# Performance work log

Hardware: AMD Instinct MI355X
Metric: run time of the kernel (lower is better)

Reference implementation:

```python
import jax, jax.numpy as jnp
import numpy as np

S = 14
B = 2
L_COORD = 5.0
L_NOOBJ = 0.5


def setup_inputs() -> dict:
    key = jax.random.key(0)
    k1, k2, k3 = jax.random.split(key, 3)
    N = 4096
    D = B * 5 + 20  # 30 channels
    pred = jax.random.uniform(k1, (N, S, S, D), dtype=jnp.float32)
    targ = jax.random.uniform(k2, (N, S, S, D), dtype=jnp.float32)
    # objectness channel of the target must be exactly 0 or 1 (loss masks on ==1 / ==0)
    obj = (jax.random.uniform(k3, (N, S, S)) < 0.15).astype(jnp.float32)
    targ = targ.at[..., 4].set(obj)
    return {"pred_tensor": pred, "target_tensor": targ}


def _yolo_loss(pred_tensor, target_tensor):
    N = pred_tensor.shape[0]
    dt = pred_tensor.dtype
    m = (target_tensor[..., 4] == 1).astype(dt)      # [N,S,S] obj mask
    nm = (target_tensor[..., 4] == 0).astype(dt)     # [N,S,S] noobj mask

    tb = target_tensor[..., :5]                                   # [N,S,S,5]
    pb = pred_tensor[..., :5 * B].reshape(N, S, S, B, 5)          # [N,S,S,B,5]

    # cell offsets: x-offset = column index j, y-offset = row index i
    ii, jj = jnp.meshgrid(jnp.arange(S, dtype=dt), jnp.arange(S, dtype=dt), indexing="ij")
    off = jnp.stack([jj, ii], axis=-1)                            # [S,S,2] = (ox, oy)

    def to_xyxy(box, off):
        # xy is scaled by 1/S, wh is NOT (faithful to the torch code)
        xy = box[..., 0:2] / S + off / S
        half = 0.5 * box[..., 2:4]
        return jnp.concatenate([xy - half, xy + half], axis=-1)

    t_xyxy = to_xyxy(tb, off)                                     # [N,S,S,4]
    p_xyxy = to_xyxy(pb, off[:, :, None, :])                      # [N,S,S,B,4]

    # per-cell IoU of target box vs each of the B predicted boxes
    lt = jnp.maximum(t_xyxy[..., None, :2], p_xyxy[..., :2])      # [N,S,S,B,2]
    rb = jnp.minimum(t_xyxy[..., None, 2:], p_xyxy[..., 2:])
    wh = jnp.clip(rb - lt, 0.0)
    inter = wh[..., 0] * wh[..., 1]                               # [N,S,S,B]
    area_t = (tb[..., 2] * tb[..., 3])[..., None]                 # [N,S,S,1]
    area_p = pb[..., 2] * pb[..., 3]                              # [N,S,S,B]
    iou = inter / (area_t + area_p - inter)                       # [N,S,S,B]

    k = jnp.argmax(iou, axis=-1)                                  # [N,S,S]
    best = jnp.take_along_axis(pb, k[..., None, None], axis=3)[..., 0, :]  # [N,S,S,5]
    best_iou = jnp.take_along_axis(iou, k[..., None], axis=-1)[..., 0]     # [N,S,S]

    loss_xy = jnp.sum(m[..., None] * (tb[..., :2] - best[..., :2]) ** 2) * L_COORD / N
    loss_wh = jnp.sum(m[..., None] * (jnp.sqrt(tb[..., 2:4]) - jnp.sqrt(best[..., 2:4])) ** 2) * L_COORD / N
    loss_Cobj = jnp.sum(m * (best_iou - best[..., 4]) ** 2) / N

    conf_sq = pb[..., 4] ** 2                                     # [N,S,S,B]
    is_best = (k[..., None] == jnp.arange(B)).astype(dt)          # [N,S,S,B]
    loss_Cnoobj = (jnp.sum(nm[..., None] * conf_sq)
                   + jnp.sum(m[..., None] * (1.0 - is_best) * conf_sq)) * L_NOOBJ / N

    loss_class = jnp.sum(m[..., None] * (target_tensor[..., 5 * B:] - pred_tensor[..., 5 * B:]) ** 2) / N

    loss_res = loss_xy + loss_wh + loss_Cobj + loss_Cnoobj + loss_class
    return (loss_res, loss_xy, loss_wh, loss_Cobj, loss_Cnoobj, loss_class)


@jax.jit
def reference(pred_tensor, target_tensor):
    return _yolo_loss(pred_tensor, target_tensor)
```

## Files before the change

kernel.cpp:

```cpp
#include <hip/hip_runtime.h>


constexpr int SS  = 14;
constexpr int TPB = 64;
constexpr int CPT = 64;
constexpr int TFL = CPT * 30;

typedef unsigned int u32;
typedef __attribute__((address_space(3))) u32 lds_u32;
typedef __attribute__((address_space(1))) const u32 glb_u32;

__device__ __forceinline__ void box_loss(
    float p0, float p1, float p2, float p3, float p4,
    float p5, float p6, float p7, float p8, float p9,
    float t0, float t1, float t2, float t3, float t4,
    float offx, float offy,
    float& s0, float& s1, float& s2, float& s3, float& m_out)
{
    float m  = (t4 == 1.0f) ? 1.0f : 0.0f;
    float nm = (t4 == 0.0f) ? 1.0f : 0.0f;
    m_out = m;

    const float S = 14.0f;
    float tcx = t0 / S + offx / S;
    float tcy = t1 / S + offy / S;
    float thw = 0.5f * t2, thh = 0.5f * t3;
    float tx0 = tcx - thw, ty0 = tcy - thh;
    float tx1 = tcx + thw, ty1 = tcy + thh;
    float area_t = t2 * t3;

    float iou0, iou1;
    {
        float cx = p0 / S + offx / S, cy = p1 / S + offy / S;
        float hw = 0.5f * p2, hh = 0.5f * p3;
        float x0 = cx - hw, y0 = cy - hh, x1 = cx + hw, y1 = cy + hh;
        float wx = fmaxf(fminf(tx1, x1) - fmaxf(tx0, x0), 0.f);
        float wy = fmaxf(fminf(ty1, y1) - fmaxf(ty0, y0), 0.f);
        float inter = wx * wy;
        iou0 = inter / (area_t + p2 * p3 - inter);
    }
    {
        float cx = p5 / S + offx / S, cy = p6 / S + offy / S;
        float hw = 0.5f * p7, hh = 0.5f * p8;
        float x0 = cx - hw, y0 = cy - hh, x1 = cx + hw, y1 = cy + hh;
        float wx = fmaxf(fminf(tx1, x1) - fmaxf(tx0, x0), 0.f);
        float wy = fmaxf(fminf(ty1, y1) - fmaxf(ty0, y0), 0.f);
        float inter = wx * wy;
        iou1 = inter / (area_t + p7 * p8 - inter);
    }

    int k = (iou1 > iou0) ? 1 : 0;
    float b0 = k ? p5 : p0, b1 = k ? p6 : p1;
    float b2 = k ? p7 : p2, b3 = k ? p8 : p3, b4 = k ? p9 : p4;
    float biou = k ? iou1 : iou0;

    float d0 = t0 - b0, d1 = t1 - b1;
    s0 += m * (d0 * d0 + d1 * d1);

    float e0 = sqrtf(t2) - sqrtf(b2);
    float e1 = sqrtf(t3) - sqrtf(b3);
    s1 += m * (e0 * e0 + e1 * e1);

    float dc = biou - b4;
    s2 += m * dc * dc;

    float conf_other = k ? p4 : p9;
    s3 += nm * (p4 * p4 + p9 * p9) + m * conf_other * conf_other;
}

__global__ __launch_bounds__(TPB) void yolo_fused(
    const float* __restrict__ pred,
    const float* __restrict__ targ,
    float4* __restrict__ partA,
    float*  __restrict__ partB,
    int ntiles)
{
    __shared__ __align__(16) float Lraw[2][2 * TFL];
    const int lane = threadIdx.x;

    float s0 = 0.f, s1 = 0.f, s2 = 0.f, s3 = 0.f, s4 = 0.f;
    const size_t tb0 = (size_t)blockIdx.x * ntiles;

    auto STAGE = [&](int buf, size_t tileIdx) {
        const float* ps = pred + tileIdx * TFL;
        const float* ts = targ + tileIdx * TFL;
        float* bp = Lraw[buf];
        float* bt = Lraw[buf] + TFL;
#pragma unroll
        for (int i = 0; i < 7; ++i)
            __builtin_amdgcn_global_load_lds((glb_u32*)(ps + i * 256 + lane * 4),
                                             (lds_u32*)(bp + i * 256), 16, 0, 0);
#pragma unroll
        for (int i = 0; i < 7; ++i)
            __builtin_amdgcn_global_load_lds((glb_u32*)(ts + i * 256 + lane * 4),
                                             (lds_u32*)(bt + i * 256), 16, 0, 0);
        if (lane < 32) {
            __builtin_amdgcn_global_load_lds((glb_u32*)(ps + 1792 + lane * 4),
                                             (lds_u32*)(bp + 1792), 16, 0, 0);
            __builtin_amdgcn_global_load_lds((glb_u32*)(ts + 1792 + lane * 4),
                                             (lds_u32*)(bt + 1792), 16, 0, 0);
        }
    };

    STAGE(0, tb0);

#pragma unroll 1
    for (int t = 0; t < ntiles; ++t) {
        if (t + 1 < ntiles) {
            STAGE((t + 1) & 1, tb0 + t + 1);
            asm volatile("s_waitcnt vmcnt(16)" ::: "memory");
        } else {
            asm volatile("s_waitcnt vmcnt(0)" ::: "memory");
        }
        __builtin_amdgcn_sched_barrier(0);

        const float* Lt = Lraw[t & 1];
        const float2* Pc = reinterpret_cast<const float2*>(Lt) + lane * 15;
        const float2* Tc = reinterpret_cast<const float2*>(Lt + TFL) + lane * 15;
        float2 a0 = Pc[0],  a1 = Pc[1],  a2 = Pc[2],  a3 = Pc[3],  a4 = Pc[4];
        float2 a5 = Pc[5],  a6 = Pc[6],  a7 = Pc[7],  a8 = Pc[8],  a9 = Pc[9];
        float2 a10 = Pc[10], a11 = Pc[11], a12 = Pc[12], a13 = Pc[13], a14 = Pc[14];
        float2 b0 = Tc[0],  b1 = Tc[1],  b2 = Tc[2];
        float2 b5 = Tc[5],  b6 = Tc[6],  b7 = Tc[7],  b8 = Tc[8],  b9 = Tc[9];
        float2 b10 = Tc[10], b11 = Tc[11], b12 = Tc[12], b13 = Tc[13], b14 = Tc[14];

        unsigned gcell = (unsigned)(tb0 + t) * CPT + (unsigned)lane;
        unsigned ij = gcell % 196u;
        float offx = (float)(ij % 14u);
        float offy = (float)(ij / 14u);

        float m;
        box_loss(a0.x, a0.y, a1.x, a1.y, a2.x, a2.y, a3.x, a3.y, a4.x, a4.y,
                 b0.x, b0.y, b1.x, b1.y, b2.x, offx, offy, s0, s1, s2, s3, m);

        float cls = 0.f, d;
        d = b5.x - a5.x;   cls += d * d;  d = b5.y - a5.y;   cls += d * d;
        d = b6.x - a6.x;   cls += d * d;  d = b6.y - a6.y;   cls += d * d;
        d = b7.x - a7.x;   cls += d * d;  d = b7.y - a7.y;   cls += d * d;
        d = b8.x - a8.x;   cls += d * d;  d = b8.y - a8.y;   cls += d * d;
        d = b9.x - a9.x;   cls += d * d;  d = b9.y - a9.y;   cls += d * d;
        d = b10.x - a10.x; cls += d * d;  d = b10.y - a10.y; cls += d * d;
        d = b11.x - a11.x; cls += d * d;  d = b11.y - a11.y; cls += d * d;
        d = b12.x - a12.x; cls += d * d;  d = b12.y - a12.y; cls += d * d;
        d = b13.x - a13.x; cls += d * d;  d = b13.y - a13.y; cls += d * d;
        d = b14.x - a14.x; cls += d * d;  d = b14.y - a14.y; cls += d * d;
        s4 += m * cls;

        asm volatile("s_waitcnt lgkmcnt(0)" ::: "memory");
        __builtin_amdgcn_sched_barrier(0);
    }

#pragma unroll
    for (int o = 32; o > 0; o >>= 1) {
        s0 += __shfl_down(s0, o);
        s1 += __shfl_down(s1, o);
        s2 += __shfl_down(s2, o);
        s3 += __shfl_down(s3, o);
        s4 += __shfl_down(s4, o);
    }
    if (lane == 0) {
        partA[blockIdx.x] = make_float4(s0, s1, s2, s3);
        partB[blockIdx.x] = s4;
    }
}

__global__ __launch_bounds__(1024) void yolo_final(
    const float4* __restrict__ partA, int nA,
    const float* __restrict__ partB,
    float* __restrict__ out, float invN)
{
    float a0 = 0.f, a1 = 0.f, a2 = 0.f, a3 = 0.f, b = 0.f;
    for (int i = threadIdx.x; i < nA; i += 1024) {
        float4 v = partA[i];
        a0 += v.x; a1 += v.y; a2 += v.z; a3 += v.w;
        b += partB[i];
    }
#pragma unroll
    for (int o = 32; o > 0; o >>= 1) {
        a0 += __shfl_down(a0, o);
        a1 += __shfl_down(a1, o);
        a2 += __shfl_down(a2, o);
        a3 += __shfl_down(a3, o);
        b  += __shfl_down(b, o);
    }
    __shared__ float red[16][5];
    int wave = threadIdx.x >> 6;
    if ((threadIdx.x & 63) == 0) {
        red[wave][0] = a0; red[wave][1] = a1; red[wave][2] = a2;
        red[wave][3] = a3; red[wave][4] = b;
    }
    __syncthreads();
    if (threadIdx.x == 0) {
        float r0 = 0, r1 = 0, r2 = 0, r3 = 0, r4 = 0;
#pragma unroll
        for (int w = 0; w < 16; ++w) {
            r0 += red[w][0]; r1 += red[w][1]; r2 += red[w][2];
            r3 += red[w][3]; r4 += red[w][4];
        }
        float xy     = r0 * 5.0f * invN;
        float wh     = r1 * 5.0f * invN;
        float cobj   = r2 * invN;
        float cnoobj = r3 * 0.5f * invN;
        float cls    = r4 * invN;
        out[0] = xy + wh + cobj + cnoobj + cls;
        out[1] = xy;
        out[2] = wh;
        out[3] = cobj;
        out[4] = cnoobj;
        out[5] = cls;
    }
}

extern "C" void kernel_launch(void* const* d_in, const int* in_sizes, int n_in,
                              void* d_out, int out_size, void* d_ws, size_t ws_size,
                              hipStream_t stream)
{
    const float* pred = (const float*)d_in[0];
    const float* targ = (const float*)d_in[1];
    int ncells = in_sizes[0] / 30;
    int ttiles = ncells / CPT;
    int N      = ncells / (SS * SS);

    int ntiles = 8;
    while ((size_t)(ttiles / ntiles) * 20 + 16 > ws_size && ntiles < 256) ntiles *= 2;
    int blocks = ttiles / ntiles;

    float4* partA = (float4*)d_ws;
    float*  partB = (float*)((char*)d_ws + (size_t)blocks * sizeof(float4));

    yolo_fused<<<blocks, TPB, 0, stream>>>(pred, targ, partA, partB, ntiles);
    yolo_final<<<1, 1024, 0, stream>>>(partA, blocks, partB,
                                       (float*)d_out, 1.0f / (float)N);
}
```

Before: 42.84 us.

## Drop LDS double buffering and launch one tile per block

Removes the double-buffered prefetch pipeline in favor of a single LDS buffer that is loaded and then waited on fully before each tile. The default tiles-per-block drops from 8 to 1, so the grid grows about eightfold and latency is hidden by having many more resident wavefronts instead of in-block prefetch. LDS per block is halved, which allows more blocks per CU. The cost is more partial sums written to the workspace and a heavier final reduction, and any block that still loops over tiles loses load/compute overlap.

```diff
diff --git a/kernel.cpp b/kernel.cpp
--- a/kernel.cpp
+++ b/kernel.cpp
@@ -75,48 +75,38 @@
     float*  __restrict__ partB,
     int ntiles)
 {
-    __shared__ __align__(16) float Lraw[2][2 * TFL];
+    __shared__ __align__(16) float Lraw[2 * TFL];
     const int lane = threadIdx.x;
 
     float s0 = 0.f, s1 = 0.f, s2 = 0.f, s3 = 0.f, s4 = 0.f;
     const size_t tb0 = (size_t)blockIdx.x * ntiles;
 
-    auto STAGE = [&](int buf, size_t tileIdx) {
-        const float* ps = pred + tileIdx * TFL;
-        const float* ts = targ + tileIdx * TFL;
-        float* bp = Lraw[buf];
-        float* bt = Lraw[buf] + TFL;
+#pragma unroll 1
+    for (int t = 0; t < ntiles; ++t) {
+        if (t) { asm volatile("s_waitcnt lgkmcnt(0)" ::: "memory");
+                 __builtin_amdgcn_sched_barrier(0); }
+
+        const float* ps = pred + (tb0 + t) * TFL;
+        const float* ts = targ + (tb0 + t) * TFL;
 #pragma unroll
         for (int i = 0; i < 7; ++i)
             __builtin_amdgcn_global_load_lds((glb_u32*)(ps + i * 256 + lane * 4),
-                                             (lds_u32*)(bp + i * 256), 16, 0, 0);
+                                             (lds_u32*)(Lraw + i * 256), 16, 0, 0);
 #pragma unroll
         for (int i = 0; i < 7; ++i)
             __builtin_amdgcn_global_load_lds((glb_u32*)(ts + i * 256 + lane * 4),
-                                             (lds_u32*)(bt + i * 256), 16, 0, 0);
+                                             (lds_u32*)(Lraw + TFL + i * 256), 16, 0, 0);
         if (lane < 32) {
             __builtin_amdgcn_global_load_lds((glb_u32*)(ps + 1792 + lane * 4),
-                                             (lds_u32*)(bp + 1792), 16, 0, 0);
+                                             (lds_u32*)(Lraw + 1792), 16, 0, 0);
             __builtin_amdgcn_global_load_lds((glb_u32*)(ts + 1792 + lane * 4),
-                                             (lds_u32*)(bt + 1792), 16, 0, 0);
+                                             (lds_u32*)(Lraw + TFL + 1792), 16, 0, 0);
         }
-    };
-
-    STAGE(0, tb0);
-
-#pragma unroll 1
-    for (int t = 0; t < ntiles; ++t) {
-        if (t + 1 < ntiles) {
-            STAGE((t + 1) & 1, tb0 + t + 1);
-            asm volatile("s_waitcnt vmcnt(16)" ::: "memory");
-        } else {
-            asm volatile("s_waitcnt vmcnt(0)" ::: "memory");
-        }
+        asm volatile("s_waitcnt vmcnt(0)" ::: "memory");
         __builtin_amdgcn_sched_barrier(0);
 
-        const float* Lt = Lraw[t & 1];
-        const float2* Pc = reinterpret_cast<const float2*>(Lt) + lane * 15;
-        const float2* Tc = reinterpret_cast<const float2*>(Lt + TFL) + lane * 15;
+        const float2* Pc = reinterpret_cast<const float2*>(Lraw) + lane * 15;
+        const float2* Tc = reinterpret_cast<const float2*>(Lraw + TFL) + lane * 15;
         float2 a0 = Pc[0],  a1 = Pc[1],  a2 = Pc[2],  a3 = Pc[3],  a4 = Pc[4];
         float2 a5 = Pc[5],  a6 = Pc[6],  a7 = Pc[7],  a8 = Pc[8],  a9 = Pc[9];
         float2 a10 = Pc[10], a11 = Pc[11], a12 = Pc[12], a13 = Pc[13], a14 = Pc[14];
@@ -145,9 +135,6 @@
         d = b13.x - a13.x; cls += d * d;  d = b13.y - a13.y; cls += d * d;
         d = b14.x - a14.x; cls += d * d;  d = b14.y - a14.y; cls += d * d;
         s4 += m * cls;
-
-        asm volatile("s_waitcnt lgkmcnt(0)" ::: "memory");
-        __builtin_amdgcn_sched_barrier(0);
     }
 
 #pragma unroll
@@ -221,7 +208,7 @@
     int ttiles = ncells / CPT;
     int N      = ncells / (SS * SS);
 
-    int ntiles = 8;
+    int ntiles = 1;
     while ((size_t)(ttiles / ntiles) * 20 + 16 > ws_size && ntiles < 256) ntiles *= 2;
     int blocks = ttiles / ntiles;
 
```

Result: faster. 39.81 us (-7.1%).
